# Kernel tuning notes

Measured on AMD Instinct MI355X. Metric: run time of the kernel, lower is better.

Reference implementation:

```python
import jax, jax.numpy as jnp
import numpy as np

N_ELEC = 4096
D_IN = 512
D_MODEL = 512
N_HEADS = 8


def setup_inputs() -> dict:
    key = jax.random.key(0)
    ks = jax.random.split(key, 6)
    scale_in = 1.0 / np.sqrt(D_IN)
    scale_model = 1.0 / np.sqrt(D_MODEL)
    return {
        "hs": jax.random.normal(ks[0], (N_ELEC, D_IN), jnp.float32),
        "hd": jax.random.normal(ks[1], (N_ELEC, D_IN), jnp.float32),
        "qk_kernel": jax.random.normal(ks[2], (D_IN, 2 * D_MODEL), jnp.float32) * scale_in,
        "qk_bias": jnp.zeros((2 * D_MODEL,), jnp.float32),
        "v_kernel": jax.random.normal(ks[3], (D_IN, D_MODEL), jnp.float32) * scale_in,
        "v_bias": jnp.zeros((D_MODEL,), jnp.float32),
        "o_kernel": jax.random.normal(ks[4], (D_MODEL, D_MODEL), jnp.float32) * scale_model,
        "o_bias": jnpp if False else jnp.zeros((D_MODEL,), jnp.float32),
    }


def reference(hs, hd, qk_kernel, qk_bias, v_kernel, v_bias, o_kernel, o_bias):
    n_elec = hs.shape[0]
    # projections
    qk = hs @ qk_kernel + qk_bias          # [N, 2*D]
    q, k = jnp.split(qk, 2, axis=-1)       # each [N, D]
    v = hd @ v_kernel + v_bias             # [N, D]
    # split heads -> [H, N, d_k]
    trans = lambda x: x.reshape(n_elec, N_HEADS, -1).transpose(1, 0, 2)
    q, k, v = trans(q), trans(k), trans(v)
    d_k = q.shape[-1]
    # scaled dot product attention (plain-array fallback path)
    logits = jnp.einsum("hnd,hmd->hnm", q, k) / jnp.sqrt(jnp.asarray(d_k, q.dtype))
    attn = jax.nn.softmax(logits, axis=-1)
    values = jnp.einsum("hnm,hmd->hnd", attn, v)   # [H, N, d_k]
    values = values.transpose(1, 0, 2).reshape(n_elec, D_MODEL)
    out = values @ o_kernel + o_bias
    return out
```

## Files before the change

kernel.cpp:

```cpp
#include <hip/hip_runtime.h>
#include <math.h>

#define N_ELEC 4096
#define DMODEL 512
#define NHEADS 8
#define DK 64

typedef __attribute__((ext_vector_type(8))) short  bf16x8;
typedef __attribute__((ext_vector_type(4))) float  f32x4;
typedef __attribute__((ext_vector_type(8))) ushort u16x8;
typedef __attribute__((ext_vector_type(4))) ushort u16x4;
typedef __attribute__((ext_vector_type(2))) unsigned int u32x2;

__device__ __forceinline__ int swz(int r, int c) { return r * 64 + (c ^ ((r & 7) * 8)); }

__device__ __forceinline__ ushort f2bf(float f) {
  union { float f; unsigned int u; } cv; cv.f = f;
  unsigned int u = cv.u;
  u += 0x7FFFu + ((u >> 16) & 1u);
  return (ushort)(u >> 16);
}

__device__ __forceinline__ unsigned cvtpk(float lo, float hi) {
  unsigned r;
  asm("v_cvt_pk_bf16_f32 %0, %1, %2" : "=v"(r) : "v"(lo), "v"(hi));
  return r;
}

#define GLL16(gp, lp) __builtin_amdgcn_global_load_lds( \
    (const __attribute__((address_space(1))) void*)(gp), \
    (__attribute__((address_space(3))) void*)(lp), 16, 0, 0)

#define QK_LOG2E 0.18033688f

__global__ __launch_bounds__(256) void prep(
    const float* __restrict__ hs, const float* __restrict__ hd,
    const float* __restrict__ qk_w, const float* __restrict__ v_w, const float* __restrict__ o_w,
    ushort* __restrict__ hsb, ushort* __restrict__ hdb,
    ushort* __restrict__ wqkT, ushort* __restrict__ wvT, ushort* __restrict__ woT)
{
  __shared__ float Ts[64][68];
  const int b = blockIdx.x, t = threadIdx.x;
  if (b < 2048) {
    const float* in = (b < 1024) ? hs : hd;
    ushort* outp = (b < 1024) ? hsb : hdb;
    const int idx = ((b & 1023) * 256 + t) * 8;
    float4 a = *(const float4*)(in + idx);
    float4 b2 = *(const float4*)(in + idx + 4);
    u16x8 o;
    o[0] = f2bf(a.x); o[1] = f2bf(a.y); o[2] = f2bf(a.z); o[3] = f2bf(a.w);
    o[4] = f2bf(b2.x); o[5] = f2bf(b2.y); o[6] = f2bf(b2.z); o[7] = f2bf(b2.w);
    *(u16x8*)(outp + idx) = o;
    return;
  }
  const float* in; ushort* outp; int C, tb;
  if (b < 2176)      { in = qk_w; outp = wqkT; C = 1024; tb = b - 2048; }
  else if (b < 2240) { in = v_w;  outp = wvT;  C = 512;  tb = b - 2176; }
  else               { in = o_w;  outp = woT;  C = 512;  tb = b - 2240; }
  const int ctiles = C >> 6;
  const int ct = (tb % ctiles) * 64, rt = (tb / ctiles) * 64;
  const int lr = t >> 4, lc4 = (t & 15) * 4;
#pragma unroll
  for (int rep = 0; rep < 4; ++rep) {
    const int r = lr + rep * 16;
    float4 v = *(const float4*)(in + (size_t)(rt + r) * C + ct + lc4);
    Ts[r][lc4] = v.x; Ts[r][lc4 + 1] = v.y; Ts[r][lc4 + 2] = v.z; Ts[r][lc4 + 3] = v.w;
  }
  __syncthreads();
#pragma unroll
  for (int rep = 0; rep < 4; ++rep) {
    const int c = lr + rep * 16;
    u16x4 o;
    o[0] = f2bf(Ts[lc4 + 0][c]); o[1] = f2bf(Ts[lc4 + 1][c]);
    o[2] = f2bf(Ts[lc4 + 2][c]); o[3] = f2bf(Ts[lc4 + 3][c]);
    *(u16x4*)(outp + (size_t)(ct + c) * 512 + rt + lc4) = o;
  }
}

template<int MODE>
__device__ __forceinline__ void proj128_body(
    ushort (&At)[2][128 * 64], ushort (&Bt)[2][128 * 64],
    const int mt, const int nt,
    const ushort* __restrict__ Wt, const ushort* __restrict__ Act,
    const float* __restrict__ bias, void* __restrict__ outp)
{
  const int t = threadIdx.x, w = t >> 6, lane = t & 63;
  const int fr = lane & 15, fp = lane >> 4;

  const ushort* rowsA = (MODE == 1) ? Act + (size_t)mt * 128 * 512 : Wt + (size_t)nt * 128 * 512;
  const ushort* rowsB = (MODE == 1) ? Wt + (size_t)nt * 128 * 512 : Act + (size_t)mt * 128 * 512;

#define STAGEP(buf, k0) do { \
  _Pragma("unroll") \
  for (int rep = 0; rep < 4; ++rep) { \
    const int cid = rep * 256 + t; \
    const int row_ = cid >> 3; \
    const int sc = ((cid & 7) ^ (row_ & 7)) * 8; \
    GLL16(rowsA + (size_t)row_ * 512 + (k0) + sc, &At[buf][(rep * 256 + w * 64) * 8]); \
    GLL16(rowsB + (size_t)row_ * 512 + (k0) + sc, &Bt[buf][(rep * 256 + w * 64) * 8]); \
  } \
} while (0)

  const int rbase = (w >> 1) * 64;
  const int cbase = (w & 1) * 64;

  f32x4 acc[16];
#pragma unroll
  for (int i = 0; i < 16; ++i) acc[i] = (f32x4){0.f, 0.f, 0.f, 0.f};

  STAGEP(0, 0);
  asm volatile("s_waitcnt vmcnt(0)" ::: "memory");
  __syncthreads();

  for (int it = 0; it < 8; ++it) {
    const int cur = it & 1;
    if (it < 7) STAGEP(cur ^ 1, (it + 1) * 64);
#pragma unroll
    for (int kh = 0; kh < 2; ++kh) {
      bf16x8 af[4], bf[4];
#pragma unroll
      for (int i = 0; i < 4; ++i) {
        af[i] = *(const bf16x8*)&At[cur][swz(rbase + i * 16 + fr, kh * 32 + fp * 8)];
        bf[i] = *(const bf16x8*)&Bt[cur][swz(cbase + i * 16 + fr, kh * 32 + fp * 8)];
      }
#pragma unroll
      for (int i = 0; i < 4; ++i)
#pragma unroll
        for (int j = 0; j < 4; ++j)
          acc[i * 4 + j] = __builtin_amdgcn_mfma_f32_16x16x32_bf16(af[i], bf[j], acc[i * 4 + j], 0, 0, 0);
    }
    asm volatile("s_waitcnt vmcnt(0)" ::: "memory");
    __syncthreads();
  }
#undef STAGEP

  if (MODE == 0) {
    ushort* out = (ushort*)outp;
#pragma unroll
    for (int i = 0; i < 4; ++i) {
      const int nb = nt * 128 + rbase + i * 16 + fp * 4;
      const float scale = (nb < 512) ? QK_LOG2E : 1.0f;
      const float4 bb = *(const float4*)(bias + nb);
      const int h = nb >> 6, d0 = nb & 63;
#pragma unroll
      for (int j = 0; j < 4; ++j) {
        const int m = mt * 128 + cbase + j * 16 + fr;
        const f32x4 a = acc[i * 4 + j];
        u16x4 o;
        o[0] = f2bf((a[0] + bb.x) * scale); o[1] = f2bf((a[1] + bb.y) * scale);
        o[2] = f2bf((a[2] + bb.z) * scale); o[3] = f2bf((a[3] + bb.w) * scale);
        *(u16x4*)(out + (size_t)h * N_ELEC * DK + (size_t)m * DK + d0) = o;
      }
    }
  } else if (MODE == 1) {
    ushort* out = (ushort*)outp;
#pragma unroll
    for (int j = 0; j < 4; ++j) {
      const int n = nt * 128 + cbase + j * 16 + fr;
      const float bb = bias[n];
      const int h = n >> 6, dd = n & 63;
#pragma unroll
      for (int i = 0; i < 4; ++i) {
        const int m0 = mt * 128 + rbase + i * 16 + fp * 4;
        const f32x4 a = acc[i * 4 + j];
        u16x4 o;
        o[0] = f2bf(a[0] + bb); o[1] = f2bf(a[1] + bb);
        o[2] = f2bf(a[2] + bb); o[3] = f2bf(a[3] + bb);
        *(u16x4*)(out + (size_t)h * DK * N_ELEC + (size_t)dd * N_ELEC + m0) = o;
      }
    }
  } else {
    float* out = (float*)outp;
#pragma unroll
    for (int i = 0; i < 4; ++i) {
      const int n0 = nt * 128 + rbase + i * 16 + fp * 4;
      const float4 bb = *(const float4*)(bias + n0);
#pragma unroll
      for (int j = 0; j < 4; ++j) {
        const int m = mt * 128 + cbase + j * 16 + fr;
        const f32x4 a = acc[i * 4 + j];
        float4 o;
        o.x = a[0] + bb.x; o.y = a[1] + bb.y; o.z = a[2] + bb.z; o.w = a[3] + bb.w;
        *(float4*)(out + (size_t)m * DMODEL + n0) = o;
      }
    }
  }
}

__global__ __launch_bounds__(256) void projQKV(
    const ushort* __restrict__ wqkT, const ushort* __restrict__ hsb,
    const ushort* __restrict__ hdb,  const ushort* __restrict__ wvT,
    const float* __restrict__ qk_b,  const float* __restrict__ v_b,
    ushort* __restrict__ qbuf, ushort* __restrict__ vbufT)
{
  __shared__ ushort At[2][128 * 64];
  __shared__ ushort Bt[2][128 * 64];
  if (blockIdx.y < 8) proj128_body<0>(At, Bt, blockIdx.x, blockIdx.y,     wqkT, hsb, qk_b, qbuf);
  else                proj128_body<1>(At, Bt, blockIdx.x, blockIdx.y - 8, wvT,  hdb, v_b,  vbufT);
}

__global__ __launch_bounds__(256) void projO(
    const ushort* __restrict__ woT, const ushort* __restrict__ Act,
    const float* __restrict__ bias, float* __restrict__ outp)
{
  __shared__ ushort At[2][128 * 64];
  __shared__ ushort Bt[2][128 * 64];
  proj128_body<2>(At, Bt, blockIdx.x, blockIdx.y, woT, Act, bias, outp);
}

template<int SPLIT>
__global__ __launch_bounds__(256, 4) void attn(
    const ushort* __restrict__ qb, const ushort* __restrict__ kb,
    const ushort* __restrict__ vtb, ushort* __restrict__ vals,
    float* __restrict__ Opart, float2* __restrict__ ML)
{
  __shared__ ushort Ks[2][64 * 64], Vts[2][64 * 64];
  __shared__ ushort Ps[4][16 * 64];
  const int bid = blockIdx.x;
  const int h = bid & 7, qt = (bid >> 3) & 31, s = bid >> 8;
  const int t = threadIdx.x, w = t >> 6, lane = t & 63;
  const int fr = lane & 15, fp = lane >> 4;
  const int KCH = N_ELEC / SPLIT;

  const ushort* kp = kb  + (size_t)h * N_ELEC * DK + (size_t)s * KCH * DK;
  const ushort* vp = vtb + (size_t)h * DK * N_ELEC + (size_t)s * KCH;
  const int q0 = qt * 128 + w * 32;

  bf16x8 qf[2][2];
#pragma unroll
  for (int qs = 0; qs < 2; ++qs) {
    const ushort* qrow = qb + (size_t)h * N_ELEC * DK + (size_t)(q0 + qs * 16 + fr) * DK + fp * 8;
    qf[qs][0] = *(const bf16x8*)(qrow);
    qf[qs][1] = *(const bf16x8*)(qrow + 32);
  }

  const int srow = lane >> 3;
  const int schunk = ((lane & 7) ^ srow) * 8;

#define STAGE(buf, j0) do { \
  _Pragma("unroll") \
  for (int p = 0; p < 2; ++p) { \
    const int rr = (w * 2 + p) * 8 + srow; \
    GLL16(kp + (size_t)((j0) + rr) * DK + schunk, &Ks[buf][(w * 2 + p) * 512]); \
    GLL16(vp + (size_t)rr * N_ELEC + (j0) + schunk, &Vts[buf][(w * 2 + p) * 512]); \
  } \
} while (0)

  float mrun[2] = {-INFINITY, -INFINITY}, lsum[2] = {0.f, 0.f};
  f32x4 oacc[2][4];
#pragma unroll
  for (int qs = 0; qs < 2; ++qs)
#pragma unroll
    for (int dt = 0; dt < 4; ++dt) oacc[qs][dt] = (f32x4){0.f, 0.f, 0.f, 0.f};

  STAGE(0, 0);
  asm volatile("s_waitcnt vmcnt(0)" ::: "memory");
  __syncthreads();

  for (int it = 0; it < KCH / 64; ++it) {
    const int cur = it & 1;
    if ((it + 1) * 64 < KCH) STAGE(cur ^ 1, (it + 1) * 64);

    f32x4 sacc[2][4];
    __builtin_amdgcn_s_setprio(1);
#pragma unroll
    for (int kt = 0; kt < 4; ++kt) {
      bf16x8 ka0 = *(const bf16x8*)&Ks[cur][swz(kt * 16 + fr, fp * 8)];
      bf16x8 ka1 = *(const bf16x8*)&Ks[cur][swz(kt * 16 + fr, fp * 8 + 32)];
#pragma unroll
      for (int qs = 0; qs < 2; ++qs) {
        f32x4 z = {0.f, 0.f, 0.f, 0.f};
        z = __builtin_amdgcn_mfma_f32_16x16x32_bf16(ka0, qf[qs][0], z, 0, 0, 0);
        sacc[qs][kt] = __builtin_amdgcn_mfma_f32_16x16x32_bf16(ka1, qf[qs][1], z, 0, 0, 0);
      }
    }
    __builtin_amdgcn_s_setprio(0);

#pragma unroll
    for (int qs = 0; qs < 2; ++qs) {
      float pm = -INFINITY;
#pragma unroll
      for (int kt = 0; kt < 4; ++kt)
#pragma unroll
        for (int g = 0; g < 4; ++g) pm = fmaxf(pm, sacc[qs][kt][g]);
      pm = fmaxf(pm, __shfl_xor(pm, 16));
      pm = fmaxf(pm, __shfl_xor(pm, 32));
      if (__any(pm > mrun[qs])) {
        const float mnew = fmaxf(mrun[qs], pm);
        const float corr = __builtin_amdgcn_exp2f(mrun[qs] - mnew);
        lsum[qs] *= corr;
#pragma unroll
        for (int dt = 0; dt < 4; ++dt) {
          oacc[qs][dt][0] *= corr; oacc[qs][dt][1] *= corr;
          oacc[qs][dt][2] *= corr; oacc[qs][dt][3] *= corr;
        }
        mrun[qs] = mnew;
      }
      float rs = 0.f;
#pragma unroll
      for (int kt = 0; kt < 4; ++kt)
#pragma unroll
        for (int g = 0; g < 4; ++g) {
          sacc[qs][kt][g] = __builtin_amdgcn_exp2f(sacc[qs][kt][g] - mrun[qs]);
          rs += sacc[qs][kt][g];
        }
      rs += __shfl_xor(rs, 16);
      rs += __shfl_xor(rs, 32);
      lsum[qs] += rs;
#pragma unroll
      for (int kt = 0; kt < 4; ++kt) {
        u32x2 pw;
        pw[0] = cvtpk(sacc[qs][kt][0], sacc[qs][kt][1]);
        pw[1] = cvtpk(sacc[qs][kt][2], sacc[qs][kt][3]);
        *(u32x2*)&Ps[w][swz(fr, kt * 16 + fp * 4)] = pw;
      }
      asm volatile("s_waitcnt lgkmcnt(0)" ::: "memory");
      bf16x8 pf0 = *(const bf16x8*)&Ps[w][swz(fr, fp * 8)];
      bf16x8 pf1 = *(const bf16x8*)&Ps[w][swz(fr, fp * 8 + 32)];
      __builtin_amdgcn_s_setprio(1);
#pragma unroll
      for (int dt = 0; dt < 4; ++dt) {
        bf16x8 v0 = *(const bf16x8*)&Vts[cur][swz(dt * 16 + fr, fp * 8)];
        bf16x8 v1 = *(const bf16x8*)&Vts[cur][swz(dt * 16 + fr, fp * 8 + 32)];
        oacc[qs][dt] = __builtin_amdgcn_mfma_f32_16x16x32_bf16(v0, pf0, oacc[qs][dt], 0, 0, 0);
        oacc[qs][dt] = __builtin_amdgcn_mfma_f32_16x16x32_bf16(v1, pf1, oacc[qs][dt], 0, 0, 0);
      }
      __builtin_amdgcn_s_setprio(0);
    }
    asm volatile("s_waitcnt vmcnt(0)" ::: "memory");
    __syncthreads();
  }
#undef STAGE

#pragma unroll
  for (int qs = 0; qs < 2; ++qs) {
    const int q = q0 + qs * 16 + fr;
    if constexpr (SPLIT == 1) {
      const float inv = 1.f / lsum[qs];
#pragma unroll
      for (int dt = 0; dt < 4; ++dt) {
        u16x4 o;
#pragma unroll
        for (int g = 0; g < 4; ++g) o[g] = f2bf(oacc[qs][dt][g] * inv);
        *(u16x4*)(vals + (size_t)q * DMODEL + h * DK + dt * 16 + fp * 4) = o;
      }
    } else {
      float* ob = Opart + ((size_t)(s * NHEADS + h) * N_ELEC + q) * DK;
#pragma unroll
      for (int dt = 0; dt < 4; ++dt) {
        float4 o;
        o.x = oacc[qs][dt][0]; o.y = oacc[qs][dt][1];
        o.z = oacc[qs][dt][2]; o.w = oacc[qs][dt][3];
        *(float4*)(ob + dt * 16 + fp * 4) = o;
      }
      if (fp == 0) ML[(size_t)(s * NHEADS + h) * N_ELEC + q] = make_float2(mrun[qs], lsum[qs]);
    }
  }
}

template<int NS>
__global__ __launch_bounds__(256) void combine(
    const float* __restrict__ Opart, const float2* __restrict__ ML,
    ushort* __restrict__ vals)
{
  const int rid = blockIdx.x * 4 + (threadIdx.x >> 6);
  const int d = threadIdx.x & 63;
  const int hh = rid >> 12, qq = rid & 4095;
  const size_t base = (size_t)rid * DK + d;
  const size_t sstride = (size_t)NHEADS * N_ELEC * DK;
  float2 mls[NS];
  float m = -INFINITY;
#pragma unroll
  for (int i = 0; i < NS; ++i) {
    mls[i] = ML[(size_t)i * NHEADS * N_ELEC + rid];
    m = fmaxf(m, mls[i].x);
  }
  float l = 0.f, o = 0.f;
#pragma unroll
  for (int i = 0; i < NS; ++i) {
    const float c = __builtin_amdgcn_exp2f(mls[i].x - m);
    l += c * mls[i].y;
    o += c * Opart[i * sstride + base];
  }
  vals[(size_t)qq * DMODEL + hh * DK + d] = f2bf(o / l);
}

extern "C" void kernel_launch(void* const* d_in, const int* in_sizes, int n_in,
                              void* d_out, int out_size, void* d_ws, size_t ws_size,
                              hipStream_t stream) {
  const float* hs   = (const float*)d_in[0];
  const float* hd   = (const float*)d_in[1];
  const float* qk_w = (const float*)d_in[2];
  const float* qk_b = (const float*)d_in[3];
  const float* v_w  = (const float*)d_in[4];
  const float* v_b  = (const float*)d_in[5];
  const float* o_w  = (const float*)d_in[6];
  const float* o_b  = (const float*)d_in[7];
  float* out = (float*)d_out;

  ushort* ws    = (ushort*)d_ws;
  ushort* hsb   = ws;
  ushort* hdb   = hsb  + (size_t)N_ELEC * DMODEL;
  ushort* wqkT  = hdb  + (size_t)N_ELEC * DMODEL;
  ushort* wvT   = wqkT + (size_t)1024 * 512;
  ushort* woT   = wvT  + (size_t)512 * 512;
  ushort* qbuf  = woT  + (size_t)512 * 512;
  ushort* kbuf  = qbuf + (size_t)NHEADS * N_ELEC * DK;
  ushort* vbufT = kbuf + (size_t)NHEADS * N_ELEC * DK;
  ushort* valsb = vbufT + (size_t)NHEADS * DK * N_ELEC;
  float*  Opart = (float*)(valsb + (size_t)N_ELEC * DMODEL);
  float2* ML4   = (float2*)(Opart + (size_t)4 * NHEADS * N_ELEC * DK);
  float2* ML2   = (float2*)(Opart + (size_t)2 * NHEADS * N_ELEC * DK);
  const size_t need4 = (size_t)((char*)(ML4 + (size_t)4 * NHEADS * N_ELEC) - (char*)d_ws);
  const size_t need2 = (size_t)((char*)(ML2 + (size_t)2 * NHEADS * N_ELEC) - (char*)d_ws);

  dim3 blk(256);
  prep<<<dim3(2304), blk, 0, stream>>>(hs, hd, qk_w, v_w, o_w, hsb, hdb, wqkT, wvT, woT);
  projQKV<<<dim3(32, 12), blk, 0, stream>>>(wqkT, hsb, hdb, wvT, qk_b, v_b, qbuf, vbufT);

  if (ws_size >= need4) {
    attn<4><<<dim3(1024), blk, 0, stream>>>(qbuf, kbuf, vbufT, nullptr, Opart, ML4);
    combine<4><<<dim3(NHEADS * N_ELEC / 4), blk, 0, stream>>>(Opart, ML4, valsb);
  } else if (ws_size >= need2) {
    attn<2><<<dim3(512), blk, 0, stream>>>(qbuf, kbuf, vbufT, nullptr, Opart, ML2);
    combine<2><<<dim3(NHEADS * N_ELEC / 4), blk, 0, stream>>>(Opart, ML2, valsb);
  } else {
    attn<1><<<dim3(256), blk, 0, stream>>>(qbuf, kbuf, vbufT, valsb, nullptr, nullptr);
  }

  projO<<<dim3(32, 4), blk, 0, stream>>>(woT, valsb, o_b, out);
}
```

Measured before the change: 102.1 us.

## Switch attention to 32x32x16 MFMA and keep P in registers via permlane swap

```diff
diff --git a/kernel.cpp b/kernel.cpp
--- a/kernel.cpp
+++ b/kernel.cpp
@@ -6,11 +6,11 @@
 #define NHEADS 8
 #define DK 64
 
-typedef __attribute__((ext_vector_type(8))) short  bf16x8;
-typedef __attribute__((ext_vector_type(4))) float  f32x4;
-typedef __attribute__((ext_vector_type(8))) ushort u16x8;
-typedef __attribute__((ext_vector_type(4))) ushort u16x4;
-typedef __attribute__((ext_vector_type(2))) unsigned int u32x2;
+typedef __attribute__((ext_vector_type(8)))  short  bf16x8;
+typedef __attribute__((ext_vector_type(4)))  float  f32x4;
+typedef __attribute__((ext_vector_type(16))) float  f32x16;
+typedef __attribute__((ext_vector_type(8)))  ushort u16x8;
+typedef __attribute__((ext_vector_type(4)))  ushort u16x4;
 
 __device__ __forceinline__ int swz(int r, int c) { return r * 64 + (c ^ ((r & 7) * 8)); }
 
@@ -26,6 +26,8 @@
   asm("v_cvt_pk_bf16_f32 %0, %1, %2" : "=v"(r) : "v"(lo), "v"(hi));
   return r;
 }
+
+#define PLSWAP(a, b) asm volatile("v_permlane32_swap_b32 %0, %1" : "+v"(a), "+v"(b))
 
 #define GLL16(gp, lp) __builtin_amdgcn_global_load_lds( \
     (const __attribute__((address_space(1))) void*)(gp), \
@@ -215,23 +217,21 @@
     float* __restrict__ Opart, float2* __restrict__ ML)
 {
   __shared__ ushort Ks[2][64 * 64], Vts[2][64 * 64];
-  __shared__ ushort Ps[4][16 * 64];
   const int bid = blockIdx.x;
   const int h = bid & 7, qt = (bid >> 3) & 31, s = bid >> 8;
   const int t = threadIdx.x, w = t >> 6, lane = t & 63;
-  const int fr = lane & 15, fp = lane >> 4;
+  const int ql = lane & 31, hi = lane >> 5;
   const int KCH = N_ELEC / SPLIT;
 
   const ushort* kp = kb  + (size_t)h * N_ELEC * DK + (size_t)s * KCH * DK;
   const ushort* vp = vtb + (size_t)h * DK * N_ELEC + (size_t)s * KCH;
-  const int q0 = qt * 128 + w * 32;
-
-  bf16x8 qf[2][2];
-#pragma unroll
-  for (int qs = 0; qs < 2; ++qs) {
-    const ushort* qrow = qb + (size_t)h * N_ELEC * DK + (size_t)(q0 + qs * 16 + fr) * DK + fp * 8;
-    qf[qs][0] = *(const bf16x8*)(qrow);
-    qf[qs][1] = *(const bf16x8*)(qrow + 32);
+  const int q = qt * 128 + w * 32 + ql;
+
+  bf16x8 qf[4];
+  {
+    const ushort* qrow = qb + (size_t)h * N_ELEC * DK + (size_t)q * DK + hi * 8;
+#pragma unroll
+    for (int kc = 0; kc < 4; ++kc) qf[kc] = *(const bf16x8*)(qrow + kc * 16);
   }
 
   const int srow = lane >> 3;
@@ -246,12 +246,10 @@
   } \
 } while (0)
 
-  float mrun[2] = {-INFINITY, -INFINITY}, lsum[2] = {0.f, 0.f};
-  f32x4 oacc[2][4];
-#pragma unroll
-  for (int qs = 0; qs < 2; ++qs)
-#pragma unroll
-    for (int dt = 0; dt < 4; ++dt) oacc[qs][dt] = (f32x4){0.f, 0.f, 0.f, 0.f};
+  float mrun = -INFINITY, lsum = 0.f;
+  f32x16 oa0, oa1;
+#pragma unroll
+  for (int i = 0; i < 16; ++i) { oa0[i] = 0.f; oa1[i] = 0.f; }
 
   STAGE(0, 0);
   asm volatile("s_waitcnt vmcnt(0)" ::: "memory");
@@ -261,100 +259,101 @@
     const int cur = it & 1;
     if ((it + 1) * 64 < KCH) STAGE(cur ^ 1, (it + 1) * 64);
 
-    f32x4 sacc[2][4];
+    f32x16 s0, s1;
+#pragma unroll
+    for (int i = 0; i < 16; ++i) { s0[i] = 0.f; s1[i] = 0.f; }
     __builtin_amdgcn_s_setprio(1);
 #pragma unroll
-    for (int kt = 0; kt < 4; ++kt) {
-      bf16x8 ka0 = *(const bf16x8*)&Ks[cur][swz(kt * 16 + fr, fp * 8)];
-      bf16x8 ka1 = *(const bf16x8*)&Ks[cur][swz(kt * 16 + fr, fp * 8 + 32)];
-#pragma unroll
-      for (int qs = 0; qs < 2; ++qs) {
-        f32x4 z = {0.f, 0.f, 0.f, 0.f};
-        z = __builtin_amdgcn_mfma_f32_16x16x32_bf16(ka0, qf[qs][0], z, 0, 0, 0);
-        sacc[qs][kt] = __builtin_amdgcn_mfma_f32_16x16x32_bf16(ka1, qf[qs][1], z, 0, 0, 0);
-      }
+    for (int kc = 0; kc < 4; ++kc) {
+      bf16x8 ka0 = *(const bf16x8*)&Ks[cur][swz(ql,      (kc * 2 + hi) * 8)];
+      bf16x8 ka1 = *(const bf16x8*)&Ks[cur][swz(32 + ql, (kc * 2 + hi) * 8)];
+      s0 = __builtin_amdgcn_mfma_f32_32x32x16_bf16(ka0, qf[kc], s0, 0, 0, 0);
+      s1 = __builtin_amdgcn_mfma_f32_32x32x16_bf16(ka1, qf[kc], s1, 0, 0, 0);
     }
     __builtin_amdgcn_s_setprio(0);
 
-#pragma unroll
-    for (int qs = 0; qs < 2; ++qs) {
-      float pm = -INFINITY;
-#pragma unroll
-      for (int kt = 0; kt < 4; ++kt)
-#pragma unroll
-        for (int g = 0; g < 4; ++g) pm = fmaxf(pm, sacc[qs][kt][g]);
-      pm = fmaxf(pm, __shfl_xor(pm, 16));
-      pm = fmaxf(pm, __shfl_xor(pm, 32));
-      if (__any(pm > mrun[qs])) {
-        const float mnew = fmaxf(mrun[qs], pm);
-        const float corr = __builtin_amdgcn_exp2f(mrun[qs] - mnew);
-        lsum[qs] *= corr;
-#pragma unroll
-        for (int dt = 0; dt < 4; ++dt) {
-          oacc[qs][dt][0] *= corr; oacc[qs][dt][1] *= corr;
-          oacc[qs][dt][2] *= corr; oacc[qs][dt][3] *= corr;
-        }
-        mrun[qs] = mnew;
-      }
-      float rs = 0.f;
-#pragma unroll
-      for (int kt = 0; kt < 4; ++kt)
-#pragma unroll
-        for (int g = 0; g < 4; ++g) {
-          sacc[qs][kt][g] = __builtin_amdgcn_exp2f(sacc[qs][kt][g] - mrun[qs]);
-          rs += sacc[qs][kt][g];
-        }
-      rs += __shfl_xor(rs, 16);
-      rs += __shfl_xor(rs, 32);
-      lsum[qs] += rs;
-#pragma unroll
-      for (int kt = 0; kt < 4; ++kt) {
-        u32x2 pw;
-        pw[0] = cvtpk(sacc[qs][kt][0], sacc[qs][kt][1]);
-        pw[1] = cvtpk(sacc[qs][kt][2], sacc[qs][kt][3]);
-        *(u32x2*)&Ps[w][swz(fr, kt * 16 + fp * 4)] = pw;
-      }
-      asm volatile("s_waitcnt lgkmcnt(0)" ::: "memory");
-      bf16x8 pf0 = *(const bf16x8*)&Ps[w][swz(fr, fp * 8)];
-      bf16x8 pf1 = *(const bf16x8*)&Ps[w][swz(fr, fp * 8 + 32)];
-      __builtin_amdgcn_s_setprio(1);
-#pragma unroll
-      for (int dt = 0; dt < 4; ++dt) {
-        bf16x8 v0 = *(const bf16x8*)&Vts[cur][swz(dt * 16 + fr, fp * 8)];
-        bf16x8 v1 = *(const bf16x8*)&Vts[cur][swz(dt * 16 + fr, fp * 8 + 32)];
-        oacc[qs][dt] = __builtin_amdgcn_mfma_f32_16x16x32_bf16(v0, pf0, oacc[qs][dt], 0, 0, 0);
-        oacc[qs][dt] = __builtin_amdgcn_mfma_f32_16x16x32_bf16(v1, pf1, oacc[qs][dt], 0, 0, 0);
-      }
-      __builtin_amdgcn_s_setprio(0);
-    }
+    float pm = -INFINITY;
+#pragma unroll
+    for (int i = 0; i < 16; ++i) pm = fmaxf(pm, fmaxf(s0[i], s1[i]));
+    pm = fmaxf(pm, __shfl_xor(pm, 32));
+    if (__any(pm > mrun)) {
+      const float mnew = fmaxf(mrun, pm);
+      const float corr = __builtin_amdgcn_exp2f(mrun - mnew);
+      lsum *= corr;
+#pragma unroll
+      for (int i = 0; i < 16; ++i) { oa0[i] *= corr; oa1[i] *= corr; }
+      mrun = mnew;
+    }
+    float rs = 0.f;
+#pragma unroll
+    for (int i = 0; i < 16; ++i) {
+      s0[i] = __builtin_amdgcn_exp2f(s0[i] - mrun); rs += s0[i];
+      s1[i] = __builtin_amdgcn_exp2f(s1[i] - mrun); rs += s1[i];
+    }
+    rs += __shfl_xor(rs, 32);
+    lsum += rs;
+
+    unsigned pb[4][4];
+#pragma unroll
+    for (int jc = 0; jc < 4; ++jc) {
+      const int base = (jc & 1) * 8;
+      unsigned A0, B0, A1, B1;
+      if (jc < 2) {
+        A0 = cvtpk(s0[base + 0], s0[base + 1]); B0 = cvtpk(s0[base + 4], s0[base + 5]);
+        A1 = cvtpk(s0[base + 2], s0[base + 3]); B1 = cvtpk(s0[base + 6], s0[base + 7]);
+      } else {
+        A0 = cvtpk(s1[base + 0], s1[base + 1]); B0 = cvtpk(s1[base + 4], s1[base + 5]);
+        A1 = cvtpk(s1[base + 2], s1[base + 3]); B1 = cvtpk(s1[base + 6], s1[base + 7]);
+      }
+      PLSWAP(A0, B0);
+      PLSWAP(A1, B1);
+      pb[jc][0] = A0; pb[jc][1] = A1; pb[jc][2] = B0; pb[jc][3] = B1;
+    }
+
+    __builtin_amdgcn_s_setprio(1);
+#pragma unroll
+    for (int jc = 0; jc < 4; ++jc) {
+      union { unsigned u[4]; bf16x8 v; } bu;
+      bu.u[0] = pb[jc][0]; bu.u[1] = pb[jc][1]; bu.u[2] = pb[jc][2]; bu.u[3] = pb[jc][3];
+      bf16x8 va0 = *(const bf16x8*)&Vts[cur][swz(ql,      (jc * 2 + hi) * 8)];
+      bf16x8 va1 = *(const bf16x8*)&Vts[cur][swz(32 + ql, (jc * 2 + hi) * 8)];
+      oa0 = __builtin_amdgcn_mfma_f32_32x32x16_bf16(va0, bu.v, oa0, 0, 0, 0);
+      oa1 = __builtin_amdgcn_mfma_f32_32x32x16_bf16(va1, bu.v, oa1, 0, 0, 0);
+    }
+    __builtin_amdgcn_s_setprio(0);
+
     asm volatile("s_waitcnt vmcnt(0)" ::: "memory");
     __syncthreads();
   }
 #undef STAGE
 
-#pragma unroll
-  for (int qs = 0; qs < 2; ++qs) {
-    const int q = q0 + qs * 16 + fr;
-    if constexpr (SPLIT == 1) {
-      const float inv = 1.f / lsum[qs];
-#pragma unroll
-      for (int dt = 0; dt < 4; ++dt) {
+  if constexpr (SPLIT == 1) {
+    const float inv = 1.f / lsum;
+#pragma unroll
+    for (int dt = 0; dt < 2; ++dt) {
+      const f32x16& oo = dt ? oa1 : oa0;
+#pragma unroll
+      for (int a = 0; a < 4; ++a) {
+        const int d0 = dt * 32 + a * 8 + hi * 4;
         u16x4 o;
 #pragma unroll
-        for (int g = 0; g < 4; ++g) o[g] = f2bf(oacc[qs][dt][g] * inv);
-        *(u16x4*)(vals + (size_t)q * DMODEL + h * DK + dt * 16 + fp * 4) = o;
-      }
-    } else {
-      float* ob = Opart + ((size_t)(s * NHEADS + h) * N_ELEC + q) * DK;
-#pragma unroll
-      for (int dt = 0; dt < 4; ++dt) {
+        for (int g = 0; g < 4; ++g) o[g] = f2bf(oo[a * 4 + g] * inv);
+        *(u16x4*)(vals + (size_t)q * DMODEL + h * DK + d0) = o;
+      }
+    }
+  } else {
+    float* ob = Opart + ((size_t)(s * NHEADS + h) * N_ELEC + q) * DK;
+#pragma unroll
+    for (int dt = 0; dt < 2; ++dt) {
+      const f32x16& oo = dt ? oa1 : oa0;
+#pragma unroll
+      for (int a = 0; a < 4; ++a) {
         float4 o;
-        o.x = oacc[qs][dt][0]; o.y = oacc[qs][dt][1];
-        o.z = oacc[qs][dt][2]; o.w = oacc[qs][dt][3];
-        *(float4*)(ob + dt * 16 + fp * 4) = o;
-      }
-      if (fp == 0) ML[(size_t)(s * NHEADS + h) * N_ELEC + q] = make_float2(mrun[qs], lsum[qs]);
-    }
+        o.x = oo[a * 4 + 0]; o.y = oo[a * 4 + 1]; o.z = oo[a * 4 + 2]; o.w = oo[a * 4 + 3];
+        *(float4*)(ob + dt * 32 + a * 8 + hi * 4) = o;
+      }
+    }
+    if (hi == 0) ML[(size_t)(s * NHEADS + h) * N_ELEC + q] = make_float2(mrun, lsum);
   }
 }
 
```

After: 102.3 us. About the same (+0.1%).
